# Kernel tuning notes

Hardware: AMD Instinct MI355X
Metric: run time of the kernel (lower is better)

The kernel has to match this reference:

```python
import jax, jax.numpy as jnp
import numpy as np

B, CIN, COUT, K, NS, NIN, H = 4, 128, 128, 9, 16384, 16384, 64
W0 = 30.0  # SIREN first-layer frequency


def setup_inputs() -> dict:
    ks = jax.random.split(jax.random.key(0), 8)
    x = jax.random.normal(ks[0], (B, CIN, NIN), dtype=jnp.float32)
    neighbours = jax.random.randint(ks[1], (K, NS), 0, NIN)
    # normalized relative neighbour coordinates in [-1, 1], shape (K*NS, 2)
    coords = 2.0 * jax.random.uniform(ks[2], (K * NS, 2), dtype=jnp.float32) - 1.0
    W1 = jax.random.normal(ks[3], (2, H), dtype=jnp.float32) / jnp.sqrt(2.0)
    b1 = jnp.zeros((H,), dtype=jnp.float32)
    W2 = jax.random.normal(ks[4], (H, H), dtype=jnp.float32) / jnp.sqrt(H * 1.0)
    b2 = jnp.zeros((H,), dtype=jnp.float32)
    W3 = jax.random.normal(ks[5], (H, COUT * CIN), dtype=jnp.float32) / jnp.sqrt(H * 1.0)
    b3 = jnp.zeros((COUT * CIN,), dtype=jnp.float32)
    bias = jnp.zeros((1, COUT, 1), dtype=jnp.float32)
    return {"x": x, "neighbours": neighbours, "coords": coords,
            "W1": W1, "b1": b1, "W2": W2, "b2": b2, "W3": W3, "b3": b3,
            "bias": bias}


def reference(x, neighbours, coords, W1, b1, W2, b2, W3, b3, bias):
    k, ns = neighbours.shape
    cin = x.shape[1]
    cout = W3.shape[1] // cin
    # INR filter generation: (K*NS, 2) -> (K*NS, COUT*CIN)
    h = jnp.sin(W0 * (coords @ W1 + b1))
    h = jnp.sin(h @ W2 + b2)
    f = h @ W3 + b3                                  # (K*NS, COUT*CIN)
    # (K*NS, COUT, CIN) -> (COUT, CIN, K, NS), matching torch permute(1,2,0).reshape
    f = f.reshape(k * ns, cout, cin).transpose(1, 2, 0).reshape(cout, cin, k, ns)
    # neighbor gather: (B, CIN, K, NS)
    x_unfold = x[:, :, neighbours]
    # weighted reduce over (CIN, K) per output location
    out = jnp.einsum('bjkl,ijkl->bil', x_unfold, f)
    return out + bias
```

## Files before the change

### kernel.cpp

```cpp
#include <hip/hip_runtime.h>

#define NS   16384
#define NIN  16384
#define CIN  128
#define COUT 128
#define KNB  9
#define MCH  66
#define QDIM (CIN*MCH)
#define W0C  30.0f

typedef __bf16 bf16;
typedef bf16  bf16x8  __attribute__((ext_vector_type(8)));
typedef float floatx4 __attribute__((ext_vector_type(4)));
typedef unsigned int u32;

__device__ inline unsigned short f2bf(float f){
  u32 u = __float_as_uint(f);
  u += 0x7fffu + ((u >> 16) & 1u);
  return (unsigned short)(u >> 16);
}
__device__ inline u32 pack2bf(float lo, float hi){
  return (u32)f2bf(lo) | ((u32)f2bf(hi) << 16);
}
__device__ inline float bf2f(unsigned short s){
  return __uint_as_float((u32)s << 16);
}

__global__ void k0_vt(const float* __restrict__ W3, const float* __restrict__ b3,
                      unsigned short* __restrict__ Vt){
  int idx = blockIdx.x*256 + threadIdx.x;
  if (idx >= COUT*QDIM) return;
  int i = idx / QDIM;
  int q = idx - i*QDIM;
  int m = q >> 7;
  int j = q & 127;
  float v = 0.f;
  if (m < 64)       v = W3[m*16384 + i*128 + j];
  else if (m == 64) v = b3[i*128 + j];
  Vt[idx] = f2bf(v);
}

__global__ __launch_bounds__(256) void k1_mlp(const float* __restrict__ coords,
      const float* __restrict__ W1, const float* __restrict__ b1,
      const float* __restrict__ W2, const float* __restrict__ b2,
      unsigned short* __restrict__ h){
  int lane = threadIdx.x & 63;
  int pt = blockIdx.x*4 + (threadIdx.x >> 6);
  float c0 = coords[2*pt], c1 = coords[2*pt+1];
  float z  = fmaf(c0, W1[lane], fmaf(c1, W1[64+lane], b1[lane]));
  float h1 = sinf(W0C * z);
  float acc = b2[lane];
  #pragma unroll
  for (int mp = 0; mp < 64; ++mp)
    acc = fmaf(__shfl(h1, mp, 64), W2[mp*64 + lane], acc);
  float h2 = sinf(acc);
  size_t base = (size_t)pt * MCH;
  h[base + lane] = f2bf(h2);
  if (lane == 0){ h[base+64] = 0x3F80; h[base+65] = 0; }
}

__global__ __launch_bounds__(256) void k1tp(const unsigned short* __restrict__ h,
                                            u32* __restrict__ hTp){
  __shared__ unsigned short t[128][68];
  int pt0 = blockIdx.x*128;
  int tid = threadIdx.x;
  for (int e = tid; e < 128*MCH; e += 256){
    int p = e / MCH, m = e - p*MCH;
    t[p][m] = h[(size_t)(pt0 + p)*MCH + m];
  }
  __syncthreads();
  for (int e = tid; e < 33*128; e += 256){
    int g = e >> 7, p = e & 127;
    hTp[(size_t)g*(KNB*NS) + pt0 + p] = (u32)t[p][2*g] | ((u32)t[p][2*g+1] << 16);
  }
}

__global__ void k_tr(const float* __restrict__ x, unsigned short* __restrict__ xT){
  __shared__ __align__(16) float t[32][33];
  int b  = blockIdx.z;
  int j0 = blockIdx.y*32;
  int p0 = blockIdx.x*32;
  int tx = threadIdx.x, ty = threadIdx.y;
  const float*    xb  = x  + (size_t)b*CIN*NIN;
  unsigned short* xTb = xT + (size_t)b*NIN*CIN;
  #pragma unroll
  for (int n = 0; n < 4; ++n)
    t[ty+8*n][tx] = xb[(size_t)(j0+ty+8*n)*NIN + p0+tx];
  __syncthreads();
  #pragma unroll
  for (int n = 0; n < 4; ++n)
    xTb[(size_t)(p0+ty+8*n)*CIN + j0+tx] = f2bf(t[tx][ty+8*n]);
}

__global__ __launch_bounds__(512, 4) void k_fused(
      const unsigned short* __restrict__ xT,
      const u32* __restrict__ hTp,
      const int* __restrict__ nb,
      const unsigned short* __restrict__ Vt,
      const float* __restrict__ bias,
      float* __restrict__ out){
  __shared__ __align__(16) unsigned short A[2][32][136];
  __shared__ u32 hm2[KNB][32];
  __shared__ int pk[KNB][32];

  const int tid = threadIdx.x;
  const int r0  = blockIdx.x * 32;
  const int b   = r0 >> 14;
  const int l0  = r0 & (NS-1);

  if (tid < KNB*32){
    int k = tid >> 5, l = tid & 31;
    pk[k][l] = nb[k*NS + l0 + l];
  }
  __syncthreads();

  const int lq = tid >> 4;
  const int jc = tid & 15;
  const char* xbB = (const char*)(xT + ((size_t)b << 21));
  bf16x8 xk[KNB];
  #pragma unroll
  for (int k = 0; k < KNB; ++k)
    xk[k] = *(const bf16x8*)(xbB + (((size_t)(u32)pk[k][lq]) << 8) + (size_t)jc*16);

  const int lane  = tid & 63;
  const int w     = tid >> 6;
  const int ar    = lane & 15;
  const int klane = lane >> 4;

  floatx4 acc[2];
  acc[0] = (floatx4){0.f,0.f,0.f,0.f};
  acc[1] = (floatx4){0.f,0.f,0.f,0.f};

  const char* VtB = (const char*)Vt + (size_t)(w*16 + ar)*(QDIM*2) + (size_t)klane*16;

  for (int mg = 0; mg < 33; ++mg){
    if (tid < KNB*32){
      int k = tid >> 5, l = tid & 31;
      hm2[k][l] = hTp[(size_t)mg*(KNB*NS) + ((size_t)k << 14) + l0 + l];
    }
    __syncthreads();

    float a2x[8], a2y[8];
    #pragma unroll
    for (int t = 0; t < 8; ++t){ a2x[t] = 0.f; a2y[t] = 0.f; }
    #pragma unroll
    for (int k = 0; k < KNB; ++k){
      u32 hw = hm2[k][lq];
      float hk0 = bf2f((unsigned short)(hw & 0xffff));
      float hk1 = bf2f((unsigned short)(hw >> 16));
      #pragma unroll
      for (int t = 0; t < 8; ++t){
        float xf = (float)xk[k][t];
        a2x[t] = fmaf(xf, hk0, a2x[t]);
        a2y[t] = fmaf(xf, hk1, a2y[t]);
      }
    }
    {
      u32 p0[4], p1[4];
      #pragma unroll
      for (int t = 0; t < 4; ++t){
        p0[t] = pack2bf(a2x[2*t], a2x[2*t+1]);
        p1[t] = pack2bf(a2y[2*t], a2y[2*t+1]);
      }
      *(uint4*)&A[0][lq][jc*8] = *(uint4*)p0;
      *(uint4*)&A[1][lq][jc*8] = *(uint4*)p1;
    }
    __syncthreads();

    #pragma unroll
    for (int mm = 0; mm < 2; ++mm){
      const char* Ab = (const char*)&A[mm][0][0] + (size_t)klane*16;
      const char* Vg = VtB + (size_t)((mg*2 + mm)*128)*2;
      #pragma unroll
      for (int kt = 0; kt < 4; ++kt){
        bf16x8 bv = *(const bf16x8*)(Vg + kt*64);
        bf16x8 av0 = *(const bf16x8*)(Ab + (0*16 + ar)*272 + kt*64);
        bf16x8 av1 = *(const bf16x8*)(Ab + (1*16 + ar)*272 + kt*64);
        acc[0] = __builtin_amdgcn_mfma_f32_16x16x32_bf16(av0, bv, acc[0], 0, 0, 0);
        acc[1] = __builtin_amdgcn_mfma_f32_16x16x32_bf16(av1, bv, acc[1], 0, 0, 0);
      }
    }
    __syncthreads();
  }

  float* ob = out + ((size_t)b << 21);
  int i = w*16 + ar;
  float bi = bias[i];
  #pragma unroll
  for (int rf = 0; rf < 2; ++rf){
    int l = l0 + rf*16 + klane*4;
    float4 v;
    v.x = acc[rf][0] + bi;
    v.y = acc[rf][1] + bi;
    v.z = acc[rf][2] + bi;
    v.w = acc[rf][3] + bi;
    *(float4*)(ob + ((size_t)i << 14) + l) = v;
  }
}

__global__ __launch_bounds__(256) void k_naive(const float* __restrict__ x,
      const int* __restrict__ nb, const float* __restrict__ coords,
      const float* __restrict__ W1, const float* __restrict__ b1,
      const float* __restrict__ W2, const float* __restrict__ b2,
      const float* __restrict__ W3, const float* __restrict__ b3,
      const float* __restrict__ bias, float* __restrict__ out){
  __shared__ __align__(16) float hk[KNB][68];
  __shared__ int pk[KNB];
  __shared__ __align__(16) float xg[4][KNB][128];
  __shared__ __align__(16) float ul[128][66];
  int tid = threadIdx.x;
  int l = blockIdx.x;
  int lane = tid & 63, wid = tid >> 6;
  if (tid < KNB) pk[tid] = nb[tid*NS + l];
  for (int k = wid; k < KNB; k += 4){
    int pt = k*NS + l;
    float c0 = coords[2*pt], c1 = coords[2*pt+1];
    float z  = fmaf(c0, W1[lane], fmaf(c1, W1[64+lane], b1[lane]));
    float h1 = sinf(W0C*z);
    float a = b2[lane];
    for (int mp = 0; mp < 64; ++mp)
      a = fmaf(__shfl(h1, mp, 64), W2[mp*64+lane], a);
    hk[k][lane] = sinf(a);
    if (lane == 0){ hk[k][64] = 1.f; hk[k][65] = 0.f; }
  }
  __syncthreads();
  for (int idx = tid; idx < 4*KNB*128; idx += 256){
    int b = idx / (KNB*128);
    int r = idx - b*KNB*128;
    int k = r >> 7;
    int j = r & 127;
    xg[b][k][j] = x[((size_t)b*CIN + j)*NIN + pk[k]];
  }
  __syncthreads();
  for (int b = 0; b < 4; ++b){
    for (int idx = tid; idx < 128*65; idx += 256){
      int j = idx / 65, m = idx - j*65;
      float s = 0.f;
      for (int k = 0; k < KNB; ++k) s = fmaf(xg[b][k][j], hk[k][m], s);
      ul[j][m] = s;
    }
    __syncthreads();
    if (tid < 128){
      int i = tid;
      float v = bias[i];
      for (int j = 0; j < 128; ++j){
        const float* wcol = W3 + i*128 + j;
        for (int m = 0; m < 64; ++m)
          v = fmaf(ul[j][m], wcol[(size_t)m*16384], v);
        v = fmaf(ul[j][64], b3[i*128+j], v);
      }
      out[((size_t)b<<21) + ((size_t)i<<14) + l] = v;
    }
    __syncthreads();
  }
}

extern "C" void kernel_launch(void* const* d_in, const int* in_sizes, int n_in,
                              void* d_out, int out_size, void* d_ws, size_t ws_size,
                              hipStream_t stream) {
  const float* x      = (const float*)d_in[0];
  const int*   nb     = (const int*)  d_in[1];
  const float* coords = (const float*)d_in[2];
  const float* W1     = (const float*)d_in[3];
  const float* b1     = (const float*)d_in[4];
  const float* W2     = (const float*)d_in[5];
  const float* b2     = (const float*)d_in[6];
  const float* W3     = (const float*)d_in[7];
  const float* b3     = (const float*)d_in[8];
  const float* bias   = (const float*)d_in[9];
  float* out = (float*)d_out;

  const size_t VT_BYTES = (size_t)COUT*QDIM*2;
  const size_t H_BYTES  = (size_t)KNB*NS*MCH*2;
  const size_t HT_BYTES = (size_t)33*KNB*NS*4;
  const size_t XT_BYTES = (size_t)4*NIN*CIN*2;
  const size_t FIXED    = VT_BYTES + H_BYTES + HT_BYTES + XT_BYTES;

  if (ws_size >= FIXED) {
    char* ws = (char*)d_ws;
    unsigned short* Vt = (unsigned short*)ws;
    unsigned short* h  = (unsigned short*)(ws + VT_BYTES);
    u32*            hTp= (u32*)(ws + VT_BYTES + H_BYTES);
    unsigned short* xT = (unsigned short*)(ws + VT_BYTES + H_BYTES + HT_BYTES);

    k0_vt<<<(COUT*QDIM + 255)/256, 256, 0, stream>>>(W3, b3, Vt);
    k1_mlp<<<(KNB*NS)/4, 256, 0, stream>>>(coords, W1, b1, W2, b2, h);
    k1tp<<<(KNB*NS)/128, 256, 0, stream>>>(h, hTp);
    k_tr<<<dim3(NIN/32, CIN/32, 4), dim3(32, 8), 0, stream>>>(x, xT);
    k_fused<<<(4*NS)/32, 512, 0, stream>>>(xT, hTp, nb, Vt, bias, out);
  } else {
    k_naive<<<NS, 256, 0, stream>>>(x, nb, coords, W1, b1, W2, b2, W3, b3, bias, out);
  }
  (void)in_sizes; (void)n_in; (void)out_size;
}
```

Baseline: 735.0 us.

## Double-buffer A tile, register-prefetch h, split-K across warps with XOR swizzle

Restructures the fused kernel main loop. The A tile is now double-buffered in shared memory with one barrier per iteration, and the h values are prefetched into registers two stages ahead instead of being staged through shared memory. Warps are reassigned to a 2x2 fragment tile per warp with the two mm halves split across warp groups, which raises B-fragment reuse; the partial sums are reduced through shared memory at the end. An XOR swizzle replaces row padding to avoid LDS bank conflicts. The cost is more accumulator registers and a final reduction pass.

```diff
diff --git a/kernel.cpp b/kernel.cpp
--- a/kernel.cpp
+++ b/kernel.cpp
@@ -99,8 +99,7 @@
       const unsigned short* __restrict__ Vt,
       const float* __restrict__ bias,
       float* __restrict__ out){
-  __shared__ __align__(16) unsigned short A[2][32][136];
-  __shared__ u32 hm2[KNB][32];
+  __shared__ __align__(16) char As[2*2*32*256];
   __shared__ int pk[KNB][32];
 
   const int tid = threadIdx.x;
@@ -108,10 +107,8 @@
   const int b   = r0 >> 14;
   const int l0  = r0 & (NS-1);
 
-  if (tid < KNB*32){
-    int k = tid >> 5, l = tid & 31;
-    pk[k][l] = nb[k*NS + l0 + l];
-  }
+  if (tid < KNB*32)
+    pk[tid >> 5][tid & 31] = nb[(tid >> 5)*NS + l0 + (tid & 31)];
   __syncthreads();
 
   const int lq = tid >> 4;
@@ -124,77 +121,137 @@
 
   const int lane  = tid & 63;
   const int w     = tid >> 6;
+  const int nc    = w & 3;
+  const int mm    = w >> 2;
   const int ar    = lane & 15;
   const int klane = lane >> 4;
 
-  floatx4 acc[2];
-  acc[0] = (floatx4){0.f,0.f,0.f,0.f};
-  acc[1] = (floatx4){0.f,0.f,0.f,0.f};
-
-  const char* VtB = (const char*)Vt + (size_t)(w*16 + ar)*(QDIM*2) + (size_t)klane*16;
-
-  for (int mg = 0; mg < 33; ++mg){
-    if (tid < KNB*32){
-      int k = tid >> 5, l = tid & 31;
-      hm2[k][l] = hTp[(size_t)mg*(KNB*NS) + ((size_t)k << 14) + l0 + l];
-    }
-    __syncthreads();
-
-    float a2x[8], a2y[8];
-    #pragma unroll
-    for (int t = 0; t < 8; ++t){ a2x[t] = 0.f; a2y[t] = 0.f; }
+  const int woff = (lq << 8) + (((jc ^ (lq & 15))) << 4);
+
+  u32 h[KNB];
+  #pragma unroll
+  for (int k = 0; k < KNB; ++k)
+    h[k] = hTp[(size_t)0*(KNB*NS) + ((size_t)k << 14) + l0 + lq];
+
+  {
+    float ax[8], ay[8];
+    #pragma unroll
+    for (int t = 0; t < 8; ++t){ ax[t] = 0.f; ay[t] = 0.f; }
     #pragma unroll
     for (int k = 0; k < KNB; ++k){
-      u32 hw = hm2[k][lq];
-      float hk0 = bf2f((unsigned short)(hw & 0xffff));
-      float hk1 = bf2f((unsigned short)(hw >> 16));
+      float hk0 = bf2f((unsigned short)(h[k] & 0xffff));
+      float hk1 = bf2f((unsigned short)(h[k] >> 16));
       #pragma unroll
       for (int t = 0; t < 8; ++t){
         float xf = (float)xk[k][t];
-        a2x[t] = fmaf(xf, hk0, a2x[t]);
-        a2y[t] = fmaf(xf, hk1, a2y[t]);
-      }
-    }
-    {
+        ax[t] = fmaf(xf, hk0, ax[t]);
+        ay[t] = fmaf(xf, hk1, ay[t]);
+      }
+    }
+    u32 p0[4], p1[4];
+    #pragma unroll
+    for (int t = 0; t < 4; ++t){
+      p0[t] = pack2bf(ax[2*t], ax[2*t+1]);
+      p1[t] = pack2bf(ay[2*t], ay[2*t+1]);
+    }
+    *(uint4*)(As + woff)        = *(uint4*)p0;
+    *(uint4*)(As + 8192 + woff) = *(uint4*)p1;
+  }
+  #pragma unroll
+  for (int k = 0; k < KNB; ++k)
+    h[k] = hTp[(size_t)1*(KNB*NS) + ((size_t)k << 14) + l0 + lq];
+  __syncthreads();
+
+  floatx4 acc[2][2];
+  #pragma unroll
+  for (int fr = 0; fr < 2; ++fr)
+    #pragma unroll
+    for (int fc = 0; fc < 2; ++fc) acc[fr][fc] = (floatx4){0.f,0.f,0.f,0.f};
+
+  const char* Vw = (const char*)Vt + (size_t)(nc*32 + ar)*(QDIM*2) + (size_t)klane*16;
+  const size_t VfcStep = (size_t)16*(QDIM*2);
+
+  for (int mg = 0; mg <= 32; ++mg){
+    const int cur = mg & 1;
+    const char* Aslab = As + cur*16384 + mm*8192;
+    const size_t qoff = (size_t)(mg*2 + mm)*256;
+    #pragma unroll
+    for (int kt = 0; kt < 4; ++kt){
+      const int ch = (((kt*4 + klane) ^ ar)) << 4;
+      bf16x8 av0 = *(const bf16x8*)(Aslab + (ar << 8) + ch);
+      bf16x8 av1 = *(const bf16x8*)(Aslab + 4096 + (ar << 8) + ch);
+      bf16x8 bv0 = *(const bf16x8*)(Vw + qoff + kt*64);
+      bf16x8 bv1 = *(const bf16x8*)(Vw + VfcStep + qoff + kt*64);
+      acc[0][0] = __builtin_amdgcn_mfma_f32_16x16x32_bf16(av0, bv0, acc[0][0], 0, 0, 0);
+      acc[0][1] = __builtin_amdgcn_mfma_f32_16x16x32_bf16(av0, bv1, acc[0][1], 0, 0, 0);
+      acc[1][0] = __builtin_amdgcn_mfma_f32_16x16x32_bf16(av1, bv0, acc[1][0], 0, 0, 0);
+      acc[1][1] = __builtin_amdgcn_mfma_f32_16x16x32_bf16(av1, bv1, acc[1][1], 0, 0, 0);
+    }
+    if (mg < 32){
+      float ax[8], ay[8];
+      #pragma unroll
+      for (int t = 0; t < 8; ++t){ ax[t] = 0.f; ay[t] = 0.f; }
+      #pragma unroll
+      for (int k = 0; k < KNB; ++k){
+        float hk0 = bf2f((unsigned short)(h[k] & 0xffff));
+        float hk1 = bf2f((unsigned short)(h[k] >> 16));
+        #pragma unroll
+        for (int t = 0; t < 8; ++t){
+          float xf = (float)xk[k][t];
+          ax[t] = fmaf(xf, hk0, ax[t]);
+          ay[t] = fmaf(xf, hk1, ay[t]);
+        }
+      }
       u32 p0[4], p1[4];
       #pragma unroll
       for (int t = 0; t < 4; ++t){
-        p0[t] = pack2bf(a2x[2*t], a2x[2*t+1]);
-        p1[t] = pack2bf(a2y[2*t], a2y[2*t+1]);
-      }
-      *(uint4*)&A[0][lq][jc*8] = *(uint4*)p0;
-      *(uint4*)&A[1][lq][jc*8] = *(uint4*)p1;
+        p0[t] = pack2bf(ax[2*t], ax[2*t+1]);
+        p1[t] = pack2bf(ay[2*t], ay[2*t+1]);
+      }
+      char* Anew = As + (cur^1)*16384;
+      *(uint4*)(Anew + woff)        = *(uint4*)p0;
+      *(uint4*)(Anew + 8192 + woff) = *(uint4*)p1;
+      if (mg < 31){
+        #pragma unroll
+        for (int k = 0; k < KNB; ++k)
+          h[k] = hTp[(size_t)(mg+2)*(KNB*NS) + ((size_t)k << 14) + l0 + lq];
+      }
     }
     __syncthreads();
-
-    #pragma unroll
-    for (int mm = 0; mm < 2; ++mm){
-      const char* Ab = (const char*)&A[mm][0][0] + (size_t)klane*16;
-      const char* Vg = VtB + (size_t)((mg*2 + mm)*128)*2;
-      #pragma unroll
-      for (int kt = 0; kt < 4; ++kt){
-        bf16x8 bv = *(const bf16x8*)(Vg + kt*64);
-        bf16x8 av0 = *(const bf16x8*)(Ab + (0*16 + ar)*272 + kt*64);
-        bf16x8 av1 = *(const bf16x8*)(Ab + (1*16 + ar)*272 + kt*64);
-        acc[0] = __builtin_amdgcn_mfma_f32_16x16x32_bf16(av0, bv, acc[0], 0, 0, 0);
-        acc[1] = __builtin_amdgcn_mfma_f32_16x16x32_bf16(av1, bv, acc[1], 0, 0, 0);
-      }
-    }
-    __syncthreads();
-  }
-
-  float* ob = out + ((size_t)b << 21);
-  int i = w*16 + ar;
-  float bi = bias[i];
-  #pragma unroll
-  for (int rf = 0; rf < 2; ++rf){
-    int l = l0 + rf*16 + klane*4;
-    float4 v;
-    v.x = acc[rf][0] + bi;
-    v.y = acc[rf][1] + bi;
-    v.z = acc[rf][2] + bi;
-    v.w = acc[rf][3] + bi;
-    *(float4*)(ob + ((size_t)i << 14) + l) = v;
+  }
+
+  float* red = (float*)As;
+  if (mm == 1){
+    #pragma unroll
+    for (int fr = 0; fr < 2; ++fr)
+      #pragma unroll
+      for (int fc = 0; fc < 2; ++fc){
+        int ii = fc*16 + ar;
+        #pragma unroll
+        for (int rg = 0; rg < 4; ++rg){
+          int li = fr*16 + klane*4 + rg;
+          red[((nc << 5) + li)*32 + ii] = acc[fr][fc][rg];
+        }
+      }
+  }
+  __syncthreads();
+  if (mm == 0){
+    float* ob = out + ((size_t)b << 21);
+    #pragma unroll
+    for (int fc = 0; fc < 2; ++fc){
+      int i = nc*32 + fc*16 + ar;
+      float bi = bias[i];
+      #pragma unroll
+      for (int fr = 0; fr < 2; ++fr){
+        int li = fr*16 + klane*4;
+        float4 v;
+        v.x = acc[fr][fc][0] + red[((nc<<5)+li+0)*32 + fc*16+ar] + bi;
+        v.y = acc[fr][fc][1] + red[((nc<<5)+li+1)*32 + fc*16+ar] + bi;
+        v.z = acc[fr][fc][2] + red[((nc<<5)+li+2)*32 + fc*16+ar] + bi;
+        v.w = acc[fr][fc][3] + red[((nc<<5)+li+3)*32 + fc*16+ar] + bi;
+        *(float4*)(ob + ((size_t)i << 14) + l0 + li) = v;
+      }
+    }
   }
 }
 
```

Result: slower. 758.0 us (+3.1%).

## Restructure fused kernel so each wave owns full 32-row tile without LDS

Applied to the files above, without the earlier changes.

The fused kernel now gives each wave a 32-location tile and all 128 output channels, looping over the CIN chunks outside and the 33 MLP-feature pairs inside. The A operand is built in registers straight into MFMA layout, which removes shared memory and all block barriers. Packing to bf16 is simplified to a single perm with rounding by adding 0x8000 instead of round-to-nearest-even. In exchange the kernel holds many more accumulator registers (16 floatx4), re-gathers x and re-reads h four times, and launches only 512 blocks, which risks low occupancy and extra memory traffic.

```diff
diff --git a/kernel.cpp b/kernel.cpp
--- a/kernel.cpp
+++ b/kernel.cpp
@@ -19,11 +19,12 @@
   u += 0x7fffu + ((u >> 16) & 1u);
   return (unsigned short)(u >> 16);
 }
-__device__ inline u32 pack2bf(float lo, float hi){
-  return (u32)f2bf(lo) | ((u32)f2bf(hi) << 16);
-}
-__device__ inline float bf2f(unsigned short s){
-  return __uint_as_float((u32)s << 16);
+__device__ inline float bf2f_lo(u32 p){ return __uint_as_float(p << 16); }
+__device__ inline float bf2f_hi(u32 p){ return __uint_as_float(p & 0xffff0000u); }
+__device__ inline u32 packbf2(float lo, float hi){
+  u32 a = __float_as_uint(lo) + 0x8000u;
+  u32 b = __float_as_uint(hi) + 0x8000u;
+  return __builtin_amdgcn_perm(b, a, 0x07060302u);
 }
 
 __global__ void k0_vt(const float* __restrict__ W3, const float* __restrict__ b3,
@@ -92,109 +93,102 @@
     xTb[(size_t)(p0+ty+8*n)*CIN + j0+tx] = f2bf(t[tx][ty+8*n]);
 }
 
-__global__ __launch_bounds__(512, 4) void k_fused(
+__global__ __launch_bounds__(256, 2) void k_fused(
       const unsigned short* __restrict__ xT,
       const u32* __restrict__ hTp,
       const int* __restrict__ nb,
       const unsigned short* __restrict__ Vt,
       const float* __restrict__ bias,
       float* __restrict__ out){
-  __shared__ __align__(16) unsigned short A[2][32][136];
-  __shared__ u32 hm2[KNB][32];
-  __shared__ int pk[KNB][32];
-
-  const int tid = threadIdx.x;
-  const int r0  = blockIdx.x * 32;
-  const int b   = r0 >> 14;
-  const int l0  = r0 & (NS-1);
-
-  if (tid < KNB*32){
-    int k = tid >> 5, l = tid & 31;
-    pk[k][l] = nb[k*NS + l0 + l];
-  }
-  __syncthreads();
-
-  const int lq = tid >> 4;
-  const int jc = tid & 15;
+  const int tid  = threadIdx.x;
+  const int lane = tid & 63;
+  const int wid  = blockIdx.x*4 + (tid >> 6);
+  const int r0   = wid << 5;
+  const int b    = r0 >> 14;
+  const int l0   = r0 & (NS-1);
+  const int ar   = lane & 15;
+  const int kl   = lane >> 4;
+
   const char* xbB = (const char*)(xT + ((size_t)b << 21));
-  bf16x8 xk[KNB];
-  #pragma unroll
-  for (int k = 0; k < KNB; ++k)
-    xk[k] = *(const bf16x8*)(xbB + (((size_t)(u32)pk[k][lq]) << 8) + (size_t)jc*16);
-
-  const int lane  = tid & 63;
-  const int w     = tid >> 6;
-  const int ar    = lane & 15;
-  const int klane = lane >> 4;
-
-  floatx4 acc[2];
-  acc[0] = (floatx4){0.f,0.f,0.f,0.f};
-  acc[1] = (floatx4){0.f,0.f,0.f,0.f};
-
-  const char* VtB = (const char*)Vt + (size_t)(w*16 + ar)*(QDIM*2) + (size_t)klane*16;
-
-  for (int mg = 0; mg < 33; ++mg){
-    if (tid < KNB*32){
-      int k = tid >> 5, l = tid & 31;
-      hm2[k][l] = hTp[(size_t)mg*(KNB*NS) + ((size_t)k << 14) + l0 + l];
-    }
-    __syncthreads();
-
-    float a2x[8], a2y[8];
+  const char* Vw  = (const char*)Vt + (size_t)ar*(QDIM*2) + (size_t)kl*16;
+
+  floatx4 acc[2][8];
+  #pragma unroll
+  for (int tl = 0; tl < 2; ++tl)
     #pragma unroll
-    for (int t = 0; t < 8; ++t){ a2x[t] = 0.f; a2y[t] = 0.f; }
+    for (int fi = 0; fi < 8; ++fi) acc[tl][fi] = (floatx4){0.f,0.f,0.f,0.f};
+
+  for (int kt = 0; kt < 4; ++kt){
+    bf16x8 x0[KNB], x1[KNB];
     #pragma unroll
     for (int k = 0; k < KNB; ++k){
-      u32 hw = hm2[k][lq];
-      float hk0 = bf2f((unsigned short)(hw & 0xffff));
-      float hk1 = bf2f((unsigned short)(hw >> 16));
-      #pragma unroll
-      for (int t = 0; t < 8; ++t){
-        float xf = (float)xk[k][t];
-        a2x[t] = fmaf(xf, hk0, a2x[t]);
-        a2y[t] = fmaf(xf, hk1, a2y[t]);
-      }
-    }
-    {
-      u32 p0[4], p1[4];
+      int p0i = nb[k*NS + l0 + ar];
+      int p1i = nb[k*NS + l0 + 16 + ar];
+      x0[k] = *(const bf16x8*)(xbB + (((size_t)(u32)p0i) << 8) + kt*64 + kl*16);
+      x1[k] = *(const bf16x8*)(xbB + (((size_t)(u32)p1i) << 8) + kt*64 + kl*16);
+    }
+
+    for (int mg = 0; mg < 33; ++mg){
+      u32 h0[KNB], h1[KNB];
+      #pragma unroll
+      for (int k = 0; k < KNB; ++k){
+        const u32* hb = hTp + (size_t)mg*(KNB*NS) + ((size_t)k << 14) + l0;
+        h0[k] = hb[ar];
+        h1[k] = hb[16 + ar];
+      }
+      float a00[8], a01[8], a10[8], a11[8];
+      #pragma unroll
+      for (int t = 0; t < 8; ++t){ a00[t]=0.f; a01[t]=0.f; a10[t]=0.f; a11[t]=0.f; }
+      #pragma unroll
+      for (int k = 0; k < KNB; ++k){
+        float h00 = bf2f_lo(h0[k]), h01 = bf2f_hi(h0[k]);
+        float h10 = bf2f_lo(h1[k]), h11 = bf2f_hi(h1[k]);
+        #pragma unroll
+        for (int t = 0; t < 8; ++t){
+          float xf0 = (float)x0[k][t];
+          float xf1 = (float)x1[k][t];
+          a00[t] = fmaf(xf0, h00, a00[t]);
+          a01[t] = fmaf(xf0, h01, a01[t]);
+          a10[t] = fmaf(xf1, h10, a10[t]);
+          a11[t] = fmaf(xf1, h11, a11[t]);
+        }
+      }
+      union AV { u32 u[4]; bf16x8 v; } av[2][2];
       #pragma unroll
       for (int t = 0; t < 4; ++t){
-        p0[t] = pack2bf(a2x[2*t], a2x[2*t+1]);
-        p1[t] = pack2bf(a2y[2*t], a2y[2*t+1]);
-      }
-      *(uint4*)&A[0][lq][jc*8] = *(uint4*)p0;
-      *(uint4*)&A[1][lq][jc*8] = *(uint4*)p1;
-    }
-    __syncthreads();
-
+        av[0][0].u[t] = packbf2(a00[2*t], a00[2*t+1]);
+        av[1][0].u[t] = packbf2(a01[2*t], a01[2*t+1]);
+        av[0][1].u[t] = packbf2(a10[2*t], a10[2*t+1]);
+        av[1][1].u[t] = packbf2(a11[2*t], a11[2*t+1]);
+      }
+      #pragma unroll
+      for (int mm = 0; mm < 2; ++mm){
+        const char* Vq = Vw + (size_t)(mg*2 + mm)*256 + kt*64;
+        #pragma unroll
+        for (int fi = 0; fi < 8; ++fi){
+          bf16x8 bv = *(const bf16x8*)(Vq + (size_t)fi*(16*QDIM*2));
+          acc[0][fi] = __builtin_amdgcn_mfma_f32_16x16x32_bf16(av[mm][0].v, bv, acc[0][fi], 0, 0, 0);
+          acc[1][fi] = __builtin_amdgcn_mfma_f32_16x16x32_bf16(av[mm][1].v, bv, acc[1][fi], 0, 0, 0);
+        }
+      }
+    }
+  }
+
+  float* ob = out + ((size_t)b << 21);
+  #pragma unroll
+  for (int fi = 0; fi < 8; ++fi){
+    int i = fi*16 + ar;
+    float bi = bias[i];
     #pragma unroll
-    for (int mm = 0; mm < 2; ++mm){
-      const char* Ab = (const char*)&A[mm][0][0] + (size_t)klane*16;
-      const char* Vg = VtB + (size_t)((mg*2 + mm)*128)*2;
-      #pragma unroll
-      for (int kt = 0; kt < 4; ++kt){
-        bf16x8 bv = *(const bf16x8*)(Vg + kt*64);
-        bf16x8 av0 = *(const bf16x8*)(Ab + (0*16 + ar)*272 + kt*64);
-        bf16x8 av1 = *(const bf16x8*)(Ab + (1*16 + ar)*272 + kt*64);
-        acc[0] = __builtin_amdgcn_mfma_f32_16x16x32_bf16(av0, bv, acc[0], 0, 0, 0);
-        acc[1] = __builtin_amdgcn_mfma_f32_16x16x32_bf16(av1, bv, acc[1], 0, 0, 0);
-      }
-    }
-    __syncthreads();
-  }
-
-  float* ob = out + ((size_t)b << 21);
-  int i = w*16 + ar;
-  float bi = bias[i];
-  #pragma unroll
-  for (int rf = 0; rf < 2; ++rf){
-    int l = l0 + rf*16 + klane*4;
-    float4 v;
-    v.x = acc[rf][0] + bi;
-    v.y = acc[rf][1] + bi;
-    v.z = acc[rf][2] + bi;
-    v.w = acc[rf][3] + bi;
-    *(float4*)(ob + ((size_t)i << 14) + l) = v;
+    for (int tl = 0; tl < 2; ++tl){
+      int l = l0 + tl*16 + kl*4;
+      float4 v;
+      v.x = acc[tl][fi][0] + bi;
+      v.y = acc[tl][fi][1] + bi;
+      v.z = acc[tl][fi][2] + bi;
+      v.w = acc[tl][fi][3] + bi;
+      *(float4*)(ob + ((size_t)i << 14) + l) = v;
+    }
   }
 }
 
@@ -287,7 +281,7 @@
     k1_mlp<<<(KNB*NS)/4, 256, 0, stream>>>(coords, W1, b1, W2, b2, h);
     k1tp<<<(KNB*NS)/128, 256, 0, stream>>>(h, hTp);
     k_tr<<<dim3(NIN/32, CIN/32, 4), dim3(32, 8), 0, stream>>>(x, xT);
-    k_fused<<<(4*NS)/32, 512, 0, stream>>>(xT, hTp, nb, Vt, bias, out);
+    k_fused<<<512, 256, 0, stream>>>(xT, hTp, nb, Vt, bias, out);
   } else {
     k_naive<<<NS, 256, 0, stream>>>(x, nb, coords, W1, b1, W2, b2, W3, b3, bias, out);
   }
```

After: 1.002 ms. 36.3% more time.
